# Performance work log

Measured on AMD Instinct MI355X. Metric: run time of the kernel, lower is better.

Reference implementation:

```python
import jax, jax.numpy as jnp
import numpy as np

B, N, DIM = 4, 4096, 512
HEADS, DIM_HEAD = 8, 64
DIM_INNER = HEADS * DIM_HEAD


def setup_inputs() -> dict:
    key = jax.random.key(0)
    k1, k2, k3 = jax.random.split(key, 3)
    x = jax.random.normal(k1, (B, N, DIM), dtype=jnp.float32)
    mask = jax.random.bernoulli(k2, 0.9, (B, N))
    W_qkv = jax.random.normal(k3, (DIM, 3 * DIM_INNER), dtype=jnp.float32) * (1.0 / np.sqrt(DIM))
    b_qkv = jnp.zeros((3 * DIM_INNER,), dtype=jnp.float32)
    return {"x": x, "mask": mask, "W_qkv": W_qkv, "b_qkv": b_qkv}


def reference(x, mask, W_qkv, b_qkv):
    # qkv projection: [b, n, 3*h*d]
    qkv = jnp.einsum('bnc,ce->bne', x, W_qkv) + b_qkv
    q, k, v = jnp.split(qkv, 3, axis=-1)

    def to_heads(t):  # b n (h d) -> b h n d
        b, n, _ = t.shape
        return t.reshape(b, n, HEADS, DIM_HEAD).transpose(0, 2, 1, 3)

    q, k, v = map(to_heads, (q, k, v))

    m = mask[:, None, :, None]  # b 1 n 1
    neg_max = -jnp.finfo(q.dtype).max
    k = jnp.where(m, k, neg_max)
    v = jnp.where(m, v, 0.0)

    k = jax.nn.softmax(k, axis=-2)  # softmax over sequence
    q = jax.nn.softmax(q, axis=-1)  # softmax over feature dim

    kv = jnp.einsum('bhnd,bhne->bhde', k, v)   # [b, h, d, d]
    out = jnp.einsum('bhde,bhnd->bhne', kv, q)  # [b, h, n, d]
    b_, h_, n_, d_ = out.shape
    return out.transpose(0, 2, 1, 3).reshape(b_, n_, h_ * d_)
```

## Files before the change

kernel.cpp:

```cpp
#include <hip/hip_runtime.h>
#include <stdint.h>

#define B_   4
#define N_   4096
#define DIM_ 512
#define H_   8
#define DH_  64
#define E3_  1536
#define M_   (B_*N_)

typedef __attribute__((ext_vector_type(8))) __bf16 bf16x8;
typedef __attribute__((ext_vector_type(8))) unsigned short ushort8;
typedef __attribute__((ext_vector_type(4))) float f32x4;

__device__ inline float bf2f(unsigned short u){ return __uint_as_float(((unsigned)u)<<16); }
__device__ inline unsigned short f2bf(float f){
  unsigned u = __float_as_uint(f);
  u += 0x7FFFu + ((u>>16)&1u);
  return (unsigned short)(u>>16);
}

__device__ inline void gld_lds16(const void* g, void* l){
  __builtin_amdgcn_global_load_lds(
      (const __attribute__((address_space(1))) void*)g,
      (__attribute__((address_space(3))) void*)l, 16, 0, 0);
}

__global__ void detect_fmt(const unsigned int* __restrict__ xw,
                           const unsigned int* __restrict__ ww,
                           const unsigned int* __restrict__ mw,
                           int* __restrict__ flags)
{
  __shared__ int cnt[2];
  __shared__ int ok[3];
  if (threadIdx.x < 2) cnt[threadIdx.x] = 0;
  if (threadIdx.x < 3) ok[threadIdx.x] = 1;
  __syncthreads();
  int hx = 0, hw = 0;
  for (int i = threadIdx.x; i < 1024; i += 256) {
    if (((xw[i] >> 7) & 0xFFu) > 140u) hx++;
    if (((ww[i] >> 7) & 0xFFu) > 140u) hw++;
  }
  int okInt = 1, okF32 = 1, okBf = 1;
  for (int i = threadIdx.x; i < 4096; i += 256) {
    unsigned w = mw[i];
    if (w > 1u) okInt = 0;
    if (w != 0u && w != 0x3F800000u) okF32 = 0;
    unsigned short a = (unsigned short)(w & 0xFFFFu), b = (unsigned short)(w >> 16);
    if (!((a == 0 || a == 0x3F80u) && (b == 0 || b == 0x3F80u))) okBf = 0;
  }
  atomicAdd(&cnt[0], hx);
  atomicAdd(&cnt[1], hw);
  if (!okInt) atomicAnd(&ok[0], 0);
  if (!okF32) atomicAnd(&ok[1], 0);
  if (!okBf)  atomicAnd(&ok[2], 0);
  __syncthreads();
  if (threadIdx.x == 0) {
    flags[0] = cnt[0] > 64 ? 1 : 0;
    flags[1] = cnt[1] > 64 ? 1 : 0;
    flags[2] = ok[0] ? 0 : (ok[1] ? 1 : (ok[2] ? 2 : 3));
  }
}

__device__ inline bool mask_at(const void* m, int flag, int idx){
  if (flag == 0) return ((const int*)m)[idx] != 0;
  if (flag == 1) return ((const float*)m)[idx] != 0.f;
  if (flag == 2) return ((const unsigned short*)m)[idx] != 0;
  return ((const unsigned char*)m)[idx] != 0;
}
__device__ inline float gread(const void* p, int f32, size_t i){
  return f32 ? ((const float*)p)[i] : bf2f(((const unsigned short*)p)[i]);
}

__device__ inline void unpack8(uint4 u, float* f){
  f[0] = bf2f((unsigned short)(u.x & 0xffff)); f[1] = bf2f((unsigned short)(u.x >> 16));
  f[2] = bf2f((unsigned short)(u.y & 0xffff)); f[3] = bf2f((unsigned short)(u.y >> 16));
  f[4] = bf2f((unsigned short)(u.z & 0xffff)); f[5] = bf2f((unsigned short)(u.z >> 16));
  f[6] = bf2f((unsigned short)(u.w & 0xffff)); f[7] = bf2f((unsigned short)(u.w >> 16));
}

__global__ __launch_bounds__(256)
void pack_xw(const void* __restrict__ x, const void* __restrict__ w,
             unsigned short* __restrict__ xq, unsigned short* __restrict__ wq,
             const int* __restrict__ flags)
{
  if (blockIdx.x < 4096) {
    const int f = flags[0];
    const int g = blockIdx.x * 256 + threadIdx.x;
    const int R = g >> 13, rem = g & 8191;
    const int kk = rem >> 9, u = rem & 511;
    const int m = R * 128 + (u & 127);
    const int k0 = kk * 32 + (u >> 7) * 8;
    ushort8 v;
    if (f) {
      const float* xp = (const float*)x + (size_t)m * DIM_ + k0;
      float4 a = *(const float4*)xp, b = *(const float4*)(xp + 4);
      v[0]=f2bf(a.x); v[1]=f2bf(a.y); v[2]=f2bf(a.z); v[3]=f2bf(a.w);
      v[4]=f2bf(b.x); v[5]=f2bf(b.y); v[6]=f2bf(b.z); v[7]=f2bf(b.w);
    } else {
      v = *(const ushort8*)((const unsigned short*)x + (size_t)m * DIM_ + k0);
    }
    *(ushort8*)&xq[(size_t)g * 8] = v;
  } else {
    const int f = flags[1];
    const int g = (blockIdx.x - 4096) * 256 + threadIdx.x;
    const int C = g >> 13, rem = g & 8191;
    const int kk = rem >> 9, u = rem & 511;
    const int n = C * 128 + (u & 127);
    const int k0 = kk * 32 + (u >> 7) * 8;
    ushort8 v;
    #pragma unroll
    for (int j = 0; j < 8; ++j) v[j] = f2bf(gread(w, f, (size_t)(k0 + j) * E3_ + n));
    *(ushort8*)&wq[(size_t)g * 8] = v;
  }
}

__global__ __launch_bounds__(512, 4)
void qkv_gemm_fused(const unsigned short* __restrict__ xq,
                    const unsigned short* __restrict__ wq,
                    const void* __restrict__ bias, const void* __restrict__ mask,
                    const int* __restrict__ flags,
                    unsigned short* __restrict__ qb,
                    unsigned short* __restrict__ ekg,
                    unsigned short* __restrict__ vmg)
{
  const int wf = flags[1], mf = flags[2];
  __shared__ alignas(16) unsigned short As[2][8192];
  __shared__ alignas(16) unsigned short Bs[2][8192];
  const int t = threadIdx.x;
  const int lane = t & 63, wv = t >> 6;
  const int quad = lane >> 4, l15 = lane & 15;
  const int m0 = blockIdx.y * 128, n0 = blockIdx.x * 128;
  const int mw = (wv & 1) * 64;
  const int nw = (wv >> 1) * 32;

  f32x4 acc[4][2];
  #pragma unroll
  for (int i = 0; i < 4; ++i)
    #pragma unroll
    for (int j = 0; j < 2; ++j) acc[i][j] = (f32x4){0.f,0.f,0.f,0.f};

  const unsigned short* aim0 = xq + ((size_t)(blockIdx.y * 16) * 512) * 8;
  const unsigned short* bim0 = wq + ((size_t)(blockIdx.x * 16) * 512) * 8;

  auto stage = [&](int kt, int bb) {
    const unsigned short* aim = aim0 + (size_t)kt * (2 * 512 * 8);
    const unsigned short* bim = bim0 + (size_t)kt * (2 * 512 * 8);
    #pragma unroll
    for (int h2 = 0; h2 < 2; ++h2) {
      const int u0 = h2 * 512 + wv * 64;
      gld_lds16(aim + (size_t)(u0 + lane) * 8, &As[bb][u0 * 8]);
      gld_lds16(bim + (size_t)(u0 + lane) * 8, &Bs[bb][u0 * 8]);
    }
  };

  stage(0, 0);
  __syncthreads();
  int cur = 0;
  for (int kt = 0; kt < 8; ++kt) {
    if (kt < 7) stage(kt + 1, cur ^ 1);
    #pragma unroll
    for (int kc = 0; kc < 2; ++kc) {
      ushort8 af[4], bfr[2];
      #pragma unroll
      for (int i = 0; i < 4; ++i)
        af[i] = *(const ushort8*)&As[cur][(kc * 512 + quad * 128 + mw + i * 16 + l15) * 8];
      #pragma unroll
      for (int j = 0; j < 2; ++j)
        bfr[j] = *(const ushort8*)&Bs[cur][(kc * 512 + quad * 128 + nw + j * 16 + l15) * 8];
      #pragma unroll
      for (int i = 0; i < 4; ++i)
        #pragma unroll
        for (int j = 0; j < 2; ++j)
          acc[i][j] = __builtin_amdgcn_mfma_f32_16x16x32_bf16(
              __builtin_bit_cast(bf16x8, af[i]), __builtin_bit_cast(bf16x8, bfr[j]),
              acc[i][j], 0, 0, 0);
    }
    __syncthreads();
    cur ^= 1;
  }

  const int mode = blockIdx.x >> 2;
  if (mode == 0) {
    #pragma unroll
    for (int j = 0; j < 2; ++j) {
      int col = n0 + nw + j * 16 + l15;
      float bv = gread(bias, wf, col);
      #pragma unroll
      for (int i = 0; i < 4; ++i)
        #pragma unroll
        for (int r = 0; r < 4; ++r) {
          int row = m0 + mw + i * 16 + quad * 4 + r;
          qb[(size_t)row * 512 + col] = f2bf(acc[i][j][r] + bv);
        }
    }
  } else {
    unsigned short* dstbuf = (mode == 1) ? ekg : vmg;
    float bj[2]; int hj[2], dj[2];
    #pragma unroll
    for (int j = 0; j < 2; ++j) {
      int col = n0 + nw + j * 16 + l15;
      bj[j] = gread(bias, wf, col);
      int rel = col - mode * 512;
      hj[j] = rel >> 6; dj[j] = rel & 63;
    }
    #pragma unroll
    for (int i = 0; i < 4; ++i)
      #pragma unroll
      for (int r = 0; r < 4; ++r) {
        int row = m0 + mw + i * 16 + quad * 4 + r;
        bool mk = mask_at(mask, mf, row);
        int bb2 = row >> 12, nn = row & 4095;
        size_t base = (size_t)(nn >> 3) * 512 + (nn & 7);
        #pragma unroll
        for (int j = 0; j < 2; ++j) {
          float val = acc[i][j][r] + bj[j];
          val = (mode == 1) ? (mk ? __expf(val) : 0.f) : (mk ? val : 0.f);
          dstbuf[(size_t)(bb2 * 8 + hj[j]) * 262144 + base + (size_t)dj[j] * 8] = f2bf(val);
        }
      }
  }
}

__global__ __launch_bounds__(256)
void kv_gemm(const unsigned short* __restrict__ ekg,
             const unsigned short* __restrict__ vmg,
             float* __restrict__ kvpart, float* __restrict__ denpart)
{
  const int sc = blockIdx.x;
  const int bh = blockIdx.y;
  const int t  = threadIdx.x;
  const int lane = t & 63, wv = t >> 6;
  const int quad = lane >> 4, l15 = lane & 15;
  __shared__ alignas(16) unsigned short ekS[16384];
  __shared__ alignas(16) unsigned short vmS[16384];

  f32x4 acc[4];
  #pragma unroll
  for (int j = 0; j < 4; ++j) acc[j] = (f32x4){0.f,0.f,0.f,0.f};
  float dsum = 0.f;
  const int dden = t & 63, g0 = (t >> 6) * 8;
  const size_t gbase = (size_t)bh * 262144 + (size_t)sc * 16384;

  #pragma unroll
  for (int i = 0; i < 8; ++i) {
    int u0 = i * 256 + wv * 64;
    gld_lds16(&ekg[gbase + (size_t)(u0 + lane) * 8], &ekS[u0 * 8]);
    gld_lds16(&vmg[gbase + (size_t)(u0 + lane) * 8], &vmS[u0 * 8]);
  }
  __syncthreads();
  {
    #pragma unroll
    for (int kt = 0; kt < 8; ++kt) {
      ushort8 v = *(const ushort8*)&ekS[((g0 + kt) * 64 + dden) * 8];
      #pragma unroll
      for (int j = 0; j < 8; ++j) dsum += bf2f(v[j]);
    }
  }
  #pragma unroll 2
  for (int ks = 0; ks < 8; ++ks) {
    ushort8 af = *(const ushort8*)&ekS[((ks * 4 + quad) * 64 + wv * 16 + l15) * 8];
    #pragma unroll
    for (int jt = 0; jt < 4; ++jt) {
      ushort8 bf8 = *(const ushort8*)&vmS[((ks * 4 + quad) * 64 + jt * 16 + l15) * 8];
      acc[jt] = __builtin_amdgcn_mfma_f32_16x16x32_bf16(
          __builtin_bit_cast(bf16x8, af), __builtin_bit_cast(bf16x8, bf8),
          acc[jt], 0, 0, 0);
    }
  }
  float* kvp = kvpart + (size_t)(sc * 32 + bh) * 4096;
  #pragma unroll
  for (int jt = 0; jt < 4; ++jt)
    #pragma unroll
    for (int r = 0; r < 4; ++r)
      kvp[(wv * 16 + quad * 4 + r) * 64 + jt * 16 + l15] = acc[jt][r];
  __syncthreads();
  float* red = (float*)ekS;
  red[t] = dsum;
  __syncthreads();
  if (t < 64)
    denpart[(sc * 32 + bh) * 64 + t] = red[t] + red[t + 64] + red[t + 128] + red[t + 192];
}

__global__ __launch_bounds__(256)
void kv_reduce(const float* __restrict__ kvpart, const float* __restrict__ denpart,
               unsigned short* __restrict__ kvnb)
{
  const int bh = blockIdx.x;
  const int qd = blockIdx.y;
  const int t  = threadIdx.x;
  __shared__ float den[16];
  if (t < 16) {
    float s = 0.f;
    #pragma unroll
    for (int c = 0; c < 16; ++c) s += denpart[(c * 32 + bh) * 64 + qd * 16 + t];
    den[t] = s;
  }
  __syncthreads();
  const int dl = t >> 4, e0 = (t & 15) * 4;
  const int d = qd * 16 + dl;
  float sx = 0.f, sy = 0.f, sz = 0.f, sw = 0.f;
  #pragma unroll
  for (int c = 0; c < 16; ++c) {
    const float4 v = *(const float4*)&kvpart[(size_t)(c * 32 + bh) * 4096 + d * 64 + e0];
    sx += v.x; sy += v.y; sz += v.z; sw += v.w;
  }
  const float inv = 1.f / den[dl];
  const float sv[4] = {sx, sy, sz, sw};
  #pragma unroll
  for (int j = 0; j < 4; ++j) {
    int e = e0 + j;
    kvnb[(size_t)bh * 4096 + ((size_t)(d >> 3) * 64 + e) * 8 + (d & 7)] = f2bf(sv[j] * inv);
  }
}

__global__ __launch_bounds__(256)
void out_pass(const unsigned short* __restrict__ qb,
              const unsigned short* __restrict__ kvnb,
              float* __restrict__ out)
{
  const int chunk = blockIdx.x, bh = blockIdx.y;
  const int b = bh >> 3, h = bh & 7;
  const int t = threadIdx.x;
  const int lane = t & 63, wv = t >> 6;
  const int quad = lane >> 4, l15 = lane & 15;
  __shared__ alignas(16) unsigned short kvS[4096];
  #pragma unroll
  for (int i = 0; i < 2; ++i)
    *(ushort8*)&kvS[(t + i * 256) * 8] =
        *(const ushort8*)&kvnb[(size_t)bh * 4096 + (size_t)(t + i * 256) * 8];
  __syncthreads();

  for (int g = 0; g < 4; ++g) {
    const int tok0 = chunk * 256 + wv * 64 + g * 16;
    const size_t qoff = (size_t)(b * N_ + tok0 + l15) * 512 + h * DH_ + quad * 8;
    uint4 qa = *(const uint4*)(qb + qoff);
    uint4 qc = *(const uint4*)(qb + qoff + 32);
    float qf[16];
    unpack8(qa, qf); unpack8(qc, qf + 8);
    float mx = qf[0];
    #pragma unroll
    for (int jj = 1; jj < 16; ++jj) mx = fmaxf(mx, qf[jj]);
    mx = fmaxf(mx, __shfl_xor(mx, 16));
    mx = fmaxf(mx, __shfl_xor(mx, 32));
    float s = 0.f;
    #pragma unroll
    for (int jj = 0; jj < 16; ++jj) { qf[jj] = __expf(qf[jj] - mx); s += qf[jj]; }
    s += __shfl_xor(s, 16);
    s += __shfl_xor(s, 32);
    const float inv = 1.f / s;
    ushort8 af0, af1;
    #pragma unroll
    for (int jj = 0; jj < 8; ++jj) {
      af0[jj] = f2bf(qf[jj] * inv);
      af1[jj] = f2bf(qf[8 + jj] * inv);
    }
    f32x4 oa[4];
    #pragma unroll
    for (int jt = 0; jt < 4; ++jt) oa[jt] = (f32x4){0.f,0.f,0.f,0.f};
    #pragma unroll
    for (int jt = 0; jt < 4; ++jt) {
      ushort8 b0 = *(const ushort8*)&kvS[((0 + quad) * 64 + jt * 16 + l15) * 8];
      ushort8 b1 = *(const ushort8*)&kvS[((4 + quad) * 64 + jt * 16 + l15) * 8];
      oa[jt] = __builtin_amdgcn_mfma_f32_16x16x32_bf16(
          __builtin_bit_cast(bf16x8, af0), __builtin_bit_cast(bf16x8, b0), oa[jt], 0, 0, 0);
      oa[jt] = __builtin_amdgcn_mfma_f32_16x16x32_bf16(
          __builtin_bit_cast(bf16x8, af1), __builtin_bit_cast(bf16x8, b1), oa[jt], 0, 0, 0);
    }
    const size_t ob = (size_t)(b * N_ + tok0 + quad * 4) * 512 + h * DH_;
    #pragma unroll
    for (int jt = 0; jt < 4; ++jt)
      #pragma unroll
      for (int r = 0; r < 4; ++r)
        out[ob + (size_t)r * 512 + jt * 16 + l15] = oa[jt][r];
  }
}

__device__ inline void stage_x_f(float (*xa)[516], const void* x, int xf, int brow0, int t)
{
  if (xf) {
    const float* xp = (const float*)x;
    #pragma unroll
    for (int s = 0; s < 8; ++s) {
      int row = (t >> 7) + 2 * s, col = (t & 127) * 4;
      *(float4*)&xa[row][col] = *(const float4*)(xp + ((size_t)(brow0 + row)) * DIM_ + col);
    }
  } else {
    const unsigned short* xp = (const unsigned short*)x;
    #pragma unroll
    for (int s = 0; s < 8; ++s) {
      int row = (t >> 7) + 2 * s, col = (t & 127) * 4;
      const unsigned short* pp = xp + ((size_t)(brow0 + row)) * DIM_ + col;
      #pragma unroll
      for (int j = 0; j < 4; ++j) xa[row][col + j] = bf2f(pp[j]);
    }
  }
}

__global__ __launch_bounds__(256)
void kv_pass_fused(const void* __restrict__ x, const void* __restrict__ w,
                   const void* __restrict__ bias, const void* __restrict__ mask,
                   const int* __restrict__ flags,
                   float* __restrict__ kvbuf, float* __restrict__ denom)
{
  const int chunk = blockIdx.x, bh = blockIdx.y;
  const int b = bh >> 3, h = bh & 7;
  const int t = threadIdx.x;
  const int xf = flags[0], wf = flags[1], mf = flags[2];
  __shared__ float xa[16][516];
  __shared__ float Wb[64][130];
  float* ekb = &Wb[0][0];
  float* vvb = &Wb[0][0] + 16 * 65;
  const int tok = t >> 4, d0 = (t & 15) * 4;
  const int down = t >> 2, e0 = (t & 3) * 16;
  float acc[16];
  #pragma unroll
  for (int i = 0; i < 16; ++i) acc[i] = 0.f;
  float dsum = 0.f;
  for (int g = 0; g < 16; ++g) {
    const int n0 = chunk * 256 + g * 16;
    __syncthreads();
    stage_x_f(xa, x, xf, b * N_ + n0, t);
    float kreg[4] = {0,0,0,0}, vreg[4] = {0,0,0,0};
    for (int cc = 0; cc < 8; ++cc) {
      __syncthreads();
      {
        int c0 = (t >> 7) * 32, col = t & 127;
        int wc = (col < 64) ? (512 + h * DH_ + col) : (1024 + h * DH_ + (col - 64));
        #pragma unroll 8
        for (int j = 0; j < 32; ++j)
          Wb[c0 + j][col] = gread(w, wf, (size_t)(cc * 64 + c0 + j) * E3_ + wc);
      }
      __syncthreads();
      #pragma unroll 4
      for (int c = 0; c < 64; ++c) {
        float xv = xa[tok][cc * 64 + c];
        #pragma unroll
        for (int j = 0; j < 4; ++j) {
          kreg[j] += xv * Wb[c][d0 + j];
          vreg[j] += xv * Wb[c][64 + d0 + j];
        }
      }
    }
    bool mk = mask_at(mask, mf, b * N_ + n0 + tok);
    __syncthreads();
    #pragma unroll
    for (int j = 0; j < 4; ++j) {
      float kvl = kreg[j] + gread(bias, wf, 512  + h * DH_ + d0 + j);
      float vvl = vreg[j] + gread(bias, wf, 1024 + h * DH_ + d0 + j);
      ekb[tok * 65 + d0 + j] = mk ? __expf(kvl) : 0.f;
      vvb[tok * 65 + d0 + j] = mk ? vvl : 0.f;
    }
    __syncthreads();
    #pragma unroll 4
    for (int nn = 0; nn < 16; ++nn) {
      float ekd = ekb[nn * 65 + down];
      if (e0 == 0) dsum += ekd;
      #pragma unroll
      for (int i = 0; i < 16; ++i) acc[i] += ekd * vvb[nn * 65 + e0 + i];
    }
  }
  float* kvp = kvbuf + (size_t)bh * 4096 + down * 64 + e0;
  #pragma unroll
  for (int i = 0; i < 16; ++i) atomicAdd(&kvp[i], acc[i]);
  if (e0 == 0) atomicAdd(&denom[bh * 64 + down], dsum);
}

__global__ __launch_bounds__(256)
void out_pass_fused(const void* __restrict__ x, const void* __restrict__ w,
                    const void* __restrict__ bias, const int* __restrict__ flags,
                    const float* __restrict__ kvbuf, const float* __restrict__ denom,
                    float* __restrict__ out)
{
  const int chunk = blockIdx.x, bh = blockIdx.y;
  const int b = bh >> 3, h = bh & 7;
  const int t = threadIdx.x;
  const int xf = flags[0], wf = flags[1];
  __shared__ float xa[16][516];
  __shared__ float Wq[64][66];
  __shared__ float kvn[64][68];
  float* qsm = &Wq[0][0];
  for (int i = t; i < 4096; i += 256) {
    int d = i >> 6, e = i & 63;
    kvn[d][e] = kvbuf[(size_t)bh * 4096 + i] / denom[bh * 64 + d];
  }
  const int tok = t >> 4, p = t & 15, d0 = p * 4;
  for (int g = 0; g < 16; ++g) {
    const int n0 = chunk * 256 + g * 16;
    __syncthreads();
    stage_x_f(xa, x, xf, b * N_ + n0, t);
    float qreg[4] = {0,0,0,0};
    for (int cc = 0; cc < 8; ++cc) {
      __syncthreads();
      {
        int col = t & 63, c0 = (t >> 6) * 16;
        #pragma unroll 8
        for (int j = 0; j < 16; ++j)
          Wq[c0 + j][col] = gread(w, wf, (size_t)(cc * 64 + c0 + j) * E3_ + h * DH_ + col);
      }
      __syncthreads();
      #pragma unroll 4
      for (int c = 0; c < 64; ++c) {
        float xv = xa[tok][cc * 64 + c];
        #pragma unroll
        for (int j = 0; j < 4; ++j) qreg[j] += xv * Wq[c][d0 + j];
      }
    }
    #pragma unroll
    for (int j = 0; j < 4; ++j) qreg[j] += gread(bias, wf, h * DH_ + d0 + j);
    float mx = fmaxf(fmaxf(qreg[0], qreg[1]), fmaxf(qreg[2], qreg[3]));
    #pragma unroll
    for (int o = 1; o < 16; o <<= 1) mx = fmaxf(mx, __shfl_xor(mx, o, 16));
    float s = 0.f;
    #pragma unroll
    for (int j = 0; j < 4; ++j) { qreg[j] = __expf(qreg[j] - mx); s += qreg[j]; }
    #pragma unroll
    for (int o = 1; o < 16; o <<= 1) s += __shfl_xor(s, o, 16);
    float inv = 1.f / s;
    __syncthreads();
    #pragma unroll
    for (int j = 0; j < 4; ++j) qsm[tok * 65 + d0 + j] = qreg[j] * inv;
    __syncthreads();
    {
      int e0 = p * 4;
      float ov[4] = {0,0,0,0};
      #pragma unroll 4
      for (int d = 0; d < 64; ++d) {
        float qd = qsm[tok * 65 + d];
        #pragma unroll
        for (int j = 0; j < 4; ++j) ov[j] += qd * kvn[d][e0 + j];
      }
      size_t ob = ((size_t)(b * N_ + n0 + tok)) * DIM_ + h * DH_ + e0;
      #pragma unroll
      for (int j = 0; j < 4; ++j) out[ob + j] = ov[j];
    }
  }
}

extern "C" void kernel_launch(void* const* d_in, const int* in_sizes, int n_in,
                              void* d_out, int out_size, void* d_ws, size_t ws_size,
                              hipStream_t stream)
{
  const void* x    = d_in[0];
  const void* mask = d_in[1];
  const void* w    = d_in[2];
  const void* bias = d_in[3];
  float* out = (float*)d_out;

  char* ws = (char*)d_ws;
  const size_t offFlg = 0;
  const size_t offXq  = 4096;
  const size_t offWq  = offXq + (size_t)M_ * DIM_ * 2;
  const size_t offQ   = offWq + (size_t)E3_ * DIM_ * 2;
  const size_t offEk  = offQ  + (size_t)M_ * DIM_ * 2;
  const size_t offVm  = offEk + (size_t)M_ * DH_ * H_ * 2;
  const size_t need   = offVm + (size_t)M_ * DH_ * H_ * 2;
  const size_t offKvp = offXq;
  const size_t offDnp = offXq + 8388608;
  const size_t offKvn = offXq + 8388608 + 131072;

  int* flags = (int*)(ws + offFlg);
  detect_fmt<<<1, 256, 0, stream>>>((const unsigned int*)x, (const unsigned int*)w,
                                    (const unsigned int*)mask, flags);

  if (ws_size >= need) {
    unsigned short* xq  = (unsigned short*)(ws + offXq);
    unsigned short* wq  = (unsigned short*)(ws + offWq);
    unsigned short* qb  = (unsigned short*)(ws + offQ);
    unsigned short* ekg = (unsigned short*)(ws + offEk);
    unsigned short* vmg = (unsigned short*)(ws + offVm);
    float* kvpart = (float*)(ws + offKvp);
    float* denpart = (float*)(ws + offDnp);
    unsigned short* kvnb = (unsigned short*)(ws + offKvn);

    pack_xw<<<4480, 256, 0, stream>>>(x, w, xq, wq, flags);
    dim3 gg(E3_ / 128, M_ / 128);
    qkv_gemm_fused<<<gg, 512, 0, stream>>>(xq, wq, bias, mask, flags, qb, ekg, vmg);
    kv_gemm<<<dim3(16, 32), 256, 0, stream>>>(ekg, vmg, kvpart, denpart);
    kv_reduce<<<dim3(32, 4), 256, 0, stream>>>(kvpart, denpart, kvnb);
    out_pass<<<dim3(16, 32), 256, 0, stream>>>(qb, kvnb, out);
  } else {
    float* kvbuf = (float*)(ws + 4096);
    float* denom = (float*)(ws + 4096 + 32 * 4096 * 4);
    hipMemsetAsync(kvbuf, 0, 32 * 4096 * 4 + 32 * 64 * 4, stream);
    dim3 ga(16, 32);
    kv_pass_fused <<<ga, 256, 0, stream>>>(x, w, bias, mask, flags, kvbuf, denom);
    out_pass_fused<<<ga, 256, 0, stream>>>(x, w, bias, flags, kvbuf, denom, out);
  }
}
```

Baseline: 181.0 us.

## Restructure QKV GEMM with 4-stage LDS pipeline, 256 threads, and block swizzle

The QKV projection GEMM moves from 512 threads with a double-buffered 64-wide K stage to 256 threads, each wave computing a 64x64 subtile, with a 4-deep ring of 32-wide K stages loaded two ahead. It uses explicit vmcnt waits and a single barrier per step. Block indices are remapped so neighbouring workgroups are spread across XCDs. The aim is more MFMA work per LDS fragment load and better overlap of global-to-LDS copies with compute, at the cost of higher register pressure and fewer waves per block.

```diff
diff --git a/kernel.cpp b/kernel.cpp
--- a/kernel.cpp
+++ b/kernel.cpp
@@ -115,7 +115,7 @@
   }
 }
 
-__global__ __launch_bounds__(512, 4)
+__global__ __launch_bounds__(256, 2)
 void qkv_gemm_fused(const unsigned short* __restrict__ xq,
                     const unsigned short* __restrict__ wq,
                     const void* __restrict__ bias, const void* __restrict__ mask,
@@ -125,65 +125,68 @@
                     unsigned short* __restrict__ vmg)
 {
   const int wf = flags[1], mf = flags[2];
-  __shared__ alignas(16) unsigned short As[2][8192];
-  __shared__ alignas(16) unsigned short Bs[2][8192];
+  __shared__ alignas(16) unsigned short As[4][4096];
+  __shared__ alignas(16) unsigned short Bs[4][4096];
   const int t = threadIdx.x;
   const int lane = t & 63, wv = t >> 6;
   const int quad = lane >> 4, l15 = lane & 15;
-  const int m0 = blockIdx.y * 128, n0 = blockIdx.x * 128;
-  const int mw = (wv & 1) * 64;
-  const int nw = (wv >> 1) * 32;
-
-  f32x4 acc[4][2];
+  const int hwf = blockIdx.y * 12 + blockIdx.x;
+  const int lf  = (hwf & 7) * 192 + (hwf >> 3);
+  const int bx = lf % 12, by = lf / 12;
+  const int m0 = by * 128, n0 = bx * 128;
+  const int mw = (wv & 1) * 64, nw = (wv >> 1) * 64;
+
+  f32x4 acc[4][4];
   #pragma unroll
   for (int i = 0; i < 4; ++i)
     #pragma unroll
-    for (int j = 0; j < 2; ++j) acc[i][j] = (f32x4){0.f,0.f,0.f,0.f};
-
-  const unsigned short* aim0 = xq + ((size_t)(blockIdx.y * 16) * 512) * 8;
-  const unsigned short* bim0 = wq + ((size_t)(blockIdx.x * 16) * 512) * 8;
-
-  auto stage = [&](int kt, int bb) {
-    const unsigned short* aim = aim0 + (size_t)kt * (2 * 512 * 8);
-    const unsigned short* bim = bim0 + (size_t)kt * (2 * 512 * 8);
-    #pragma unroll
-    for (int h2 = 0; h2 < 2; ++h2) {
-      const int u0 = h2 * 512 + wv * 64;
+    for (int j = 0; j < 4; ++j) acc[i][j] = (f32x4){0.f,0.f,0.f,0.f};
+
+  const unsigned short* aim0 = xq + ((size_t)(by * 16) * 512) * 8;
+  const unsigned short* bim0 = wq + ((size_t)(bx * 16) * 512) * 8;
+
+  auto stage = [&](int kk, int bb) {
+    const unsigned short* aim = aim0 + (size_t)kk * 4096;
+    const unsigned short* bim = bim0 + (size_t)kk * 4096;
+    #pragma unroll
+    for (int s = 0; s < 2; ++s) {
+      const int u0 = s * 256 + wv * 64;
       gld_lds16(aim + (size_t)(u0 + lane) * 8, &As[bb][u0 * 8]);
       gld_lds16(bim + (size_t)(u0 + lane) * 8, &Bs[bb][u0 * 8]);
     }
   };
 
   stage(0, 0);
-  __syncthreads();
-  int cur = 0;
-  for (int kt = 0; kt < 8; ++kt) {
-    if (kt < 7) stage(kt + 1, cur ^ 1);
-    #pragma unroll
-    for (int kc = 0; kc < 2; ++kc) {
-      ushort8 af[4], bfr[2];
-      #pragma unroll
-      for (int i = 0; i < 4; ++i)
-        af[i] = *(const ushort8*)&As[cur][(kc * 512 + quad * 128 + mw + i * 16 + l15) * 8];
-      #pragma unroll
-      for (int j = 0; j < 2; ++j)
-        bfr[j] = *(const ushort8*)&Bs[cur][(kc * 512 + quad * 128 + nw + j * 16 + l15) * 8];
-      #pragma unroll
-      for (int i = 0; i < 4; ++i)
-        #pragma unroll
-        for (int j = 0; j < 2; ++j)
-          acc[i][j] = __builtin_amdgcn_mfma_f32_16x16x32_bf16(
-              __builtin_bit_cast(bf16x8, af[i]), __builtin_bit_cast(bf16x8, bfr[j]),
-              acc[i][j], 0, 0, 0);
-    }
-    __syncthreads();
-    cur ^= 1;
-  }
-
-  const int mode = blockIdx.x >> 2;
+  stage(1, 1);
+  #pragma unroll
+  for (int kk = 0; kk < 16; ++kk) {
+    const int bb = kk & 3;
+    if (kk < 14) stage(kk + 2, (kk + 2) & 3);
+    if (kk < 14)       asm volatile("s_waitcnt vmcnt(8)" ::: "memory");
+    else if (kk == 14) asm volatile("s_waitcnt vmcnt(4)" ::: "memory");
+    else               asm volatile("s_waitcnt vmcnt(0)" ::: "memory");
+    __builtin_amdgcn_sched_barrier(0);
+    __builtin_amdgcn_s_barrier();
+    __builtin_amdgcn_sched_barrier(0);
+    ushort8 af[4], bfr[4];
+    #pragma unroll
+    for (int i = 0; i < 4; ++i) {
+      af[i]  = *(const ushort8*)&As[bb][(quad * 128 + mw + i * 16 + l15) * 8];
+      bfr[i] = *(const ushort8*)&Bs[bb][(quad * 128 + nw + i * 16 + l15) * 8];
+    }
+    #pragma unroll
+    for (int i = 0; i < 4; ++i)
+      #pragma unroll
+      for (int j = 0; j < 4; ++j)
+        acc[i][j] = __builtin_amdgcn_mfma_f32_16x16x32_bf16(
+            __builtin_bit_cast(bf16x8, af[i]), __builtin_bit_cast(bf16x8, bfr[j]),
+            acc[i][j], 0, 0, 0);
+  }
+
+  const int mode = bx >> 2;
   if (mode == 0) {
     #pragma unroll
-    for (int j = 0; j < 2; ++j) {
+    for (int j = 0; j < 4; ++j) {
       int col = n0 + nw + j * 16 + l15;
       float bv = gread(bias, wf, col);
       #pragma unroll
@@ -196,9 +199,9 @@
     }
   } else {
     unsigned short* dstbuf = (mode == 1) ? ekg : vmg;
-    float bj[2]; int hj[2], dj[2];
-    #pragma unroll
-    for (int j = 0; j < 2; ++j) {
+    float bj[4]; int hj[4], dj[4];
+    #pragma unroll
+    for (int j = 0; j < 4; ++j) {
       int col = n0 + nw + j * 16 + l15;
       bj[j] = gread(bias, wf, col);
       int rel = col - mode * 512;
@@ -213,7 +216,7 @@
         int bb2 = row >> 12, nn = row & 4095;
         size_t base = (size_t)(nn >> 3) * 512 + (nn & 7);
         #pragma unroll
-        for (int j = 0; j < 2; ++j) {
+        for (int j = 0; j < 4; ++j) {
           float val = acc[i][j][r] + bj[j];
           val = (mode == 1) ? (mk ? __expf(val) : 0.f) : (mk ? val : 0.f);
           dstbuf[(size_t)(bb2 * 8 + hj[j]) * 262144 + base + (size_t)dj[j] * 8] = f2bf(val);
@@ -575,7 +578,7 @@
 
     pack_xw<<<4480, 256, 0, stream>>>(x, w, xq, wq, flags);
     dim3 gg(E3_ / 128, M_ / 128);
-    qkv_gemm_fused<<<gg, 512, 0, stream>>>(xq, wq, bias, mask, flags, qb, ekg, vmg);
+    qkv_gemm_fused<<<gg, 256, 0, stream>>>(xq, wq, bias, mask, flags, qb, ekg, vmg);
     kv_gemm<<<dim3(16, 32), 256, 0, stream>>>(ekg, vmg, kvpart, denpart);
     kv_reduce<<<dim3(32, 4), 256, 0, stream>>>(kvpart, denpart, kvnb);
     out_pass<<<dim3(16, 32), 256, 0, stream>>>(qb, kvnb, out);
```

Result: faster. 173.4 us (median of 2 runs) (-4.2%).
